# Optimization experiments

Hardware: AMD Instinct MI355X
Metric: run time of the kernel (lower is better)

## Reference

```python
import jax, jax.numpy as jnp
import numpy as np

K = 3  # PyG TAGConv default number of hops


def _gcn_norm(edge_index, num_nodes):
    # Symmetric GCN normalization WITHOUT self-loops (TAGConv default).
    row, col = edge_index[0], edge_index[1]
    w = jnp.ones(edge_index.shape[1], dtype=jnp.float32)
    deg = jax.ops.segment_sum(w, col, num_segments=num_nodes)
    dinv = jnp.where(deg > 0, jax.lax.rsqrt(jnp.maximum(deg, 1.0)), 0.0)
    return dinv[row] * dinv[col]  # [E]


def _tagconv(x, edge_index, norm, W, b):
    # W: [K+1, d_in, d_out], b: [d_out]
    row, col = edge_index[0], edge_index[1]
    n = x.shape[0]
    out = x @ W[0]
    h = x
    for k in range(1, K + 1):
        # h <- D^-1/2 A D^-1/2 h  via gather + segment-sum scatter
        h = jax.ops.segment_sum(norm[:, None] * h[row], col, num_segments=n)
        out = out + h @ W[k]
    return out + b


def setup_inputs() -> dict:
    key = jax.random.key(0)
    k1, k2, k3, k4, k5, k6 = jax.random.split(key, 6)
    N, E = 100000, 1600000
    d_in, d_hid, d_out = 64, 64, 40
    x = jax.random.normal(k1, (N, d_in), dtype=jnp.float32)
    edge_index = jax.random.randint(k2, (2, E), 0, N, dtype=jnp.int32)
    s1 = 1.0 / np.sqrt(d_in)
    s2 = 1.0 / np.sqrt(d_hid)
    W1 = jax.random.uniform(k3, (K + 1, d_in, d_hid), jnp.float32, -s1, s1)
    b1 = jnp.zeros((d_hid,), jnp.float32)
    W2 = jax.random.uniform(k4, (K + 1, d_hid, d_out), jnp.float32, -s2, s2)
    b2 = jnp.zeros((d_out,), jnp.float32)
    return {"x": x, "edge_index": edge_index, "W1": W1, "b1": b1, "W2": W2, "b2": b2}


def reference(x, edge_index, W1, b1, W2, b2):
    norm = _gcn_norm(edge_index, x.shape[0])
    h = jax.nn.relu(_tagconv(x, edge_index, norm, W1, b1))
    # F.dropout in eval mode: identity
    h = _tagconv(h, edge_index, norm, W2, b2)
    return jax.nn.log_softmax(h, axis=1)
```

## Files before the change

### kernel.cpp

```cpp
#include <hip/hip_runtime.h>
#include <math.h>

#define DIN 64
#define NB_MAX 512
#define S1_CHUNK 4096

typedef unsigned short us8 __attribute__((ext_vector_type(8)));
typedef short s16x8 __attribute__((ext_vector_type(8)));
typedef float f32x4 __attribute__((ext_vector_type(4)));


__device__ __forceinline__ float bf2f(unsigned short u) {
    return __uint_as_float(((unsigned int)u) << 16);
}
__device__ __forceinline__ unsigned short f2bf(float f) {
    unsigned int u = __float_as_uint(f);
    return (unsigned short)((u + 0x7fffu + ((u >> 16) & 1u)) >> 16);
}


__global__ __launch_bounds__(256) void bcount_kernel(const int* __restrict__ col,
                                                     int* __restrict__ bcnt, int E, int NB) {
    __shared__ int cntB[NB_MAX];
    for (int t = threadIdx.x; t < NB; t += 256) cntB[t] = 0;
    __syncthreads();
    int stride = gridDim.x * blockDim.x;
    for (int i = blockIdx.x * blockDim.x + threadIdx.x; i < E; i += stride)
        atomicAdd(&cntB[col[i] >> 8], 1);
    __syncthreads();
    for (int t = threadIdx.x; t < NB; t += 256) {
        int c = cntB[t];
        if (c) atomicAdd(&bcnt[t], c);
    }
}

__global__ void bscan_kernel(const int* __restrict__ bcnt, int* __restrict__ bbase,
                             int* __restrict__ gcur, int* __restrict__ rowptr,
                             int NB, int N, int E) {
    __shared__ int sm[512];
    int tid = threadIdx.x;
    int v = (tid < NB) ? bcnt[tid] : 0;
    sm[tid] = v;
    __syncthreads();
    for (int off = 1; off < 512; off <<= 1) {
        int add = (tid >= off) ? sm[tid - off] : 0;
        __syncthreads();
        sm[tid] += add;
        __syncthreads();
    }
    if (tid < NB) { int b = sm[tid] - v; bbase[tid] = b; gcur[tid] = b; }
    if (tid == NB - 1) bbase[NB] = sm[tid];
    if (tid == 0) rowptr[N] = E;
}


__global__ __launch_bounds__(256) void s1_bucket(const int* __restrict__ row,
                                                 const int* __restrict__ col,
                                                 int* __restrict__ gcur,
                                                 int* __restrict__ sorted, int E, int NB) {
    __shared__ int2 ebuf[S1_CHUNK];
    __shared__ int cntL[NB_MAX];
    __shared__ int baseL[NB_MAX];
    __shared__ int curL[NB_MAX];
    __shared__ int gbaseL[NB_MAX];
    __shared__ int sm[256];
    int tid = threadIdx.x;
    int jb = blockIdx.x * S1_CHUNK;
    int je = min(jb + S1_CHUNK, E);
    int cntTot = je - jb;

    for (int t = tid; t < NB; t += 256) cntL[t] = 0;
    __syncthreads();
    for (int j = jb + tid; j < je; j += 256) atomicAdd(&cntL[col[j] >> 8], 1);
    __syncthreads();
    int per = (NB + 255) >> 8;
    int s = 0;
    for (int q = 0; q < per; ++q) {
        int idx = tid * per + q;
        if (idx < NB) s += cntL[idx];
    }
    sm[tid] = s;
    __syncthreads();
    for (int off = 1; off < 256; off <<= 1) {
        int add = (tid >= off) ? sm[tid - off] : 0;
        __syncthreads();
        sm[tid] += add;
        __syncthreads();
    }
    int run = sm[tid] - s;
    for (int q = 0; q < per; ++q) {
        int idx = tid * per + q;
        if (idx < NB) { baseL[idx] = run; curL[idx] = run; run += cntL[idx]; }
    }
    __syncthreads();
    for (int t = tid; t < NB; t += 256)
        gbaseL[t] = atomicAdd(&gcur[t], cntL[t]);
    for (int j = jb + tid; j < je; j += 256) {
        int c = col[j];
        int pos = atomicAdd(&curL[c >> 8], 1);
        ebuf[pos] = make_int2(row[j], c);
    }
    __syncthreads();
    for (int jj = tid; jj < cntTot; jj += 256) {
        int2 e = ebuf[jj];
        int t = e.y >> 8;
        sorted[gbaseL[t] + (jj - baseL[t])] = (e.x << 8) | (e.y & 255);
    }
}


__global__ __launch_bounds__(256) void s2_kernel(const int* __restrict__ sorted,
                                                 const int* __restrict__ bbase,
                                                 int* __restrict__ rowptr,
                                                 float* __restrict__ dinv,
                                                 float* __restrict__ rdinv,
                                                 int* __restrict__ srcarr, int N) {
    __shared__ int cntL[256], baseL[256], sm[256];
    int tid = threadIdx.x;
    int b = blockIdx.x;
    int c0 = b << 8;
    int nLoc = min(256, N - c0);
    int gs = bbase[b], ge = bbase[b + 1];
    cntL[tid] = 0;
    __syncthreads();
    for (int j = gs + tid; j < ge; j += 256)
        atomicAdd(&cntL[sorted[j] & 255], 1);
    __syncthreads();
    int c = cntL[tid];
    sm[tid] = c;
    __syncthreads();
    for (int off = 1; off < 256; off <<= 1) {
        int add = (tid >= off) ? sm[tid - off] : 0;
        __syncthreads();
        sm[tid] += add;
        __syncthreads();
    }
    int base = gs + sm[tid] - c;
    baseL[tid] = base;
    if (tid < nLoc) {
        rowptr[c0 + tid] = base;
        dinv[c0 + tid] = (c > 0) ? rsqrtf((float)c) : 0.0f;
        rdinv[c0 + tid] = (c > 0) ? sqrtf((float)c) : 0.0f;
    }
    cntL[tid] = 0;
    __syncthreads();
    for (int j = gs + tid; j < ge; j += 256) {
        int e = sorted[j];
        int cl = e & 255;
        int p = baseL[cl] + atomicAdd(&cntL[cl], 1);
        srcarr[p] = e >> 8;
    }
}


__global__ void cvt_kernel(const float* __restrict__ x, const float* __restrict__ dinv,
                           unsigned short* __restrict__ hb0, unsigned short* __restrict__ sb0,
                           int n4) {
    int i = blockIdx.x * blockDim.x + threadIdx.x;
    if (i >= n4) return;
    float d = dinv[i >> 4];
    float4 v = *(const float4*)&x[(size_t)i * 4];
    ushort4 h, s;
    h.x = f2bf(v.x); h.y = f2bf(v.y); h.z = f2bf(v.z); h.w = f2bf(v.w);
    s.x = f2bf(d * v.x); s.y = f2bf(d * v.y); s.z = f2bf(d * v.z); s.w = f2bf(d * v.w);
    *(ushort4*)&hb0[(size_t)i * 4] = h;
    *(ushort4*)&sb0[(size_t)i * 4] = s;
}


__global__ __launch_bounds__(256) void prop_kernel(const int* __restrict__ rowptr,
                                                   const int* __restrict__ srcarr,
                                                   const float* __restrict__ dinv,
                                                   const unsigned short* __restrict__ sb_in,
                                                   unsigned short* __restrict__ sb_out, int N) {
    int gid = blockIdx.x * blockDim.x + threadIdx.x;
    int node = gid >> 6;
    if (node >= N) return;
    int lane = threadIdx.x & 63;
    int g = lane >> 3, l = lane & 7;
    int beg = rowptr[node], end = rowptr[node + 1];
    int deg = end - beg;
    float a[8] = {};
    for (int chunk = 0; chunk < deg; chunk += 64) {
        int lim = min(64, deg - chunk);
        int src_l = (lane < lim) ? srcarr[beg + chunk + lane] : 0;
        int iters = (lim + 7) >> 3;
        for (int t = 0; t < iters; ++t) {
            int jj = g + (t << 3);
            int src = __shfl(src_l, jj, 64);
            if (jj < lim) {
                us8 hv = *(const us8*)&sb_in[(size_t)src * DIN + l * 8];
#pragma unroll
                for (int k = 0; k < 8; ++k) a[k] += bf2f(hv[k]);
            }
        }
    }
#pragma unroll
    for (int off = 8; off < 64; off <<= 1) {
#pragma unroll
        for (int k = 0; k < 8; ++k) a[k] += __shfl_xor(a[k], off, 64);
    }
    if (g == 0) {
        float d = dinv[node];
        float d2 = d * d;
        us8 o;
#pragma unroll
        for (int k = 0; k < 8; ++k) o[k] = f2bf(d2 * a[k]);
        *(us8*)&sb_out[(size_t)node * DIN + l * 8] = o;
    }
}


__global__ void wprep_kernel(const float* __restrict__ W, unsigned short* __restrict__ Wb,
                             int DOUTsrc, int CT) {
    int idx = blockIdx.x * blockDim.x + threadIdx.x;
    int total = 4 * 2 * CT * 64;
    if (idx >= total) return;
    int lane = idx & 63;
    int rest = idx >> 6;
    int ct = rest % CT;
    int tmp = rest / CT;
    int ks = tmp & 1, kk = tmp >> 1;
    int colc = ct * 16 + (lane & 15);
    int k0 = ks * 32 + (lane >> 4) * 8;
    us8 ov;
#pragma unroll
    for (int j = 0; j < 8; ++j) {
        float v = (colc < DOUTsrc) ? W[(size_t)(kk * 64 + k0 + j) * DOUTsrc + colc] : 0.0f;
        ov[j] = f2bf(v);
    }
    *(us8*)&Wb[(size_t)idx * 8] = ov;
}


template <int CT, int MODE>
__global__ __launch_bounds__(256) void mm4m_kernel(const unsigned short* __restrict__ h0,
                                                   const unsigned short* __restrict__ s1,
                                                   const unsigned short* __restrict__ s2,
                                                   const unsigned short* __restrict__ s3,
                                                   const float* __restrict__ rdinv,
                                                   const float* __restrict__ dinv,
                                                   const unsigned short* __restrict__ Wb,
                                                   const float* __restrict__ bias,
                                                   float* __restrict__ outf,
                                                   unsigned short* __restrict__ outh,
                                                   unsigned short* __restrict__ outs, int N) {
    constexpr int LSTR = (MODE == 2) ? 68 : 52;
    __shared__ __align__(16) float Lds[64 * LSTR];
    int tid = threadIdx.x;
    int w = tid >> 6, lane = tid & 63;
    int row0 = blockIdx.x * 64 + w * 16;
    int arow = row0 + (lane & 15);
    bool aok = arow < N;
    size_t abase = (size_t)arow * DIN + ((lane >> 4) * 8);
    const unsigned short* hp[4] = {h0, s1, s2, s3};

    f32x4 acc0[CT] = {};
    f32x4 accS[CT] = {};
#pragma unroll
    for (int kk = 0; kk < 4; ++kk) {
        const unsigned short* hb = hp[kk];
#pragma unroll
        for (int ks = 0; ks < 2; ++ks) {
            s16x8 a = {};
            if (aok) a = *(const s16x8*)&hb[abase + ks * 32];
#pragma unroll
            for (int c = 0; c < CT; ++c) {
                s16x8 b = *(const s16x8*)&Wb[(size_t)(((kk * 2 + ks) * CT + c) * 64 + lane) * 8];
                if (kk == 0)
                    acc0[c] = __builtin_amdgcn_mfma_f32_16x16x32_bf16(a, b, acc0[c], 0, 0, 0);
                else
                    accS[c] = __builtin_amdgcn_mfma_f32_16x16x32_bf16(a, b, accS[c], 0, 0, 0);
            }
        }
    }
    int lcol = lane & 15;
    int lrow4 = (lane >> 4) * 4;
#pragma unroll
    for (int r = 0; r < 4; ++r) {
        int lr = lrow4 + r;
        int grow = row0 + lr;
        float rd = (grow < N) ? rdinv[grow] : 0.0f;
#pragma unroll
        for (int c = 0; c < CT; ++c) {
            float v = acc0[c][r] + rd * accS[c][r];
            if (MODE == 2) {
                v += bias[c * 16 + lcol];
                v = v > 0.0f ? v : 0.0f;
            }
            Lds[(w * 16 + lr) * LSTR + c * 16 + lcol] = v;
        }
    }
    __syncthreads();
    int rowsInBlk = min(64, N - blockIdx.x * 64);
    if (MODE == 2) {
        for (int idx = tid; idx < rowsInBlk * 8; idx += 256) {
            int r = idx >> 3, k8 = (idx & 7) * 8;
            int gr = blockIdx.x * 64 + r;
            float d = dinv[gr];
            us8 oh, os;
#pragma unroll
            for (int k = 0; k < 8; ++k) {
                float v = Lds[r * LSTR + k8 + k];
                oh[k] = f2bf(v);
                os[k] = f2bf(d * v);
            }
            *(us8*)&outh[(size_t)gr * DIN + k8] = oh;
            *(us8*)&outs[(size_t)gr * DIN + k8] = os;
        }
    } else {
        for (int idx = tid; idx < rowsInBlk * 10; idx += 256) {
            int r = idx / 10, c4 = idx - r * 10;
            int gr = blockIdx.x * 64 + r;
            float4 v = *(float4*)&Lds[r * LSTR + c4 * 4];
            *(float4*)&outf[(size_t)gr * 40 + c4 * 4] = v;
        }
    }
}


__global__ void lsm_kernel(float* __restrict__ out, const float* __restrict__ bias, int N) {
    int gid = blockIdx.x * blockDim.x + threadIdx.x;
    int row = gid >> 6;
    int lane = gid & 63;
    if (row >= N) return;
    float v = (lane < 40) ? out[(size_t)row * 40 + lane] + bias[lane] : -INFINITY;
    float m = v;
    for (int off = 32; off > 0; off >>= 1) m = fmaxf(m, __shfl_xor(m, off, 64));
    float e = (lane < 40) ? expf(v - m) : 0.0f;
    float ssum = e;
    for (int off = 32; off > 0; off >>= 1) ssum += __shfl_xor(ssum, off, 64);
    if (lane < 40) out[(size_t)row * 40 + lane] = v - m - logf(ssum);
}


extern "C" void kernel_launch(void* const* d_in, const int* in_sizes, int n_in,
                              void* d_out, int out_size, void* d_ws, size_t ws_size,
                              hipStream_t stream) {
    const float* x  = (const float*)d_in[0];
    const int*   ei = (const int*)d_in[1];
    const float* W1 = (const float*)d_in[2];
    const float* b1 = (const float*)d_in[3];
    const float* W2 = (const float*)d_in[4];
    const float* b2 = (const float*)d_in[5];

    int N = in_sizes[0] / DIN;
    int E = in_sizes[1] / 2;
    const int* rowv = ei;
    const int* colv = ei + E;
    int NB = (N + 255) >> 8;

    char* p = (char*)d_ws;
    auto alloc = [&](size_t bytes) {
        char* q = p;
        p += (bytes + 255) & ~(size_t)255;
        return q;
    };
    int*   bcnt   = (int*)alloc(NB_MAX * 4);
    int*   bbase  = (int*)alloc((NB_MAX + 1) * 4);
    int*   gcur   = (int*)alloc(NB_MAX * 4);
    int*   rowptr = (int*)alloc((size_t)(N + 1) * 4);
    float* dinv   = (float*)alloc((size_t)N * 4);
    float* rdinv  = (float*)alloc((size_t)N * 4);
    int*   sorted = (int*)alloc((size_t)E * 4);
    int*   srcarr = (int*)alloc((size_t)E * 4);
    unsigned short* Wb1 = (unsigned short*)alloc((size_t)4 * 2 * 4 * 64 * 8 * 2);
    unsigned short* Wb2 = (unsigned short*)alloc((size_t)4 * 2 * 3 * 64 * 8 * 2);
    unsigned short* hb0 = (unsigned short*)alloc((size_t)N * DIN * 2);
    unsigned short* hbE = (unsigned short*)alloc((size_t)N * DIN * 2);
    unsigned short* sbA = (unsigned short*)alloc((size_t)N * DIN * 2);
    unsigned short* sbB = (unsigned short*)alloc((size_t)N * DIN * 2);
    unsigned short* sbC = (unsigned short*)alloc((size_t)N * DIN * 2);
    unsigned short* sbD = (unsigned short*)alloc((size_t)N * DIN * 2);
    float* outp   = (float*)d_out;

    hipMemsetAsync(bcnt, 0, NB_MAX * 4, stream);

    const int tpb = 256;

    bcount_kernel<<<128, tpb, 0, stream>>>(colv, bcnt, E, NB);
    bscan_kernel<<<1, 512, 0, stream>>>(bcnt, bbase, gcur, rowptr, NB, N, E);
    s1_bucket<<<(E + S1_CHUNK - 1) / S1_CHUNK, 256, 0, stream>>>(rowv, colv, gcur, sorted, E, NB);
    s2_kernel<<<NB, 256, 0, stream>>>(sorted, bbase, rowptr, dinv, rdinv, srcarr, N);
    wprep_kernel<<<8, tpb, 0, stream>>>(W1, Wb1, 64, 4);
    wprep_kernel<<<6, tpb, 0, stream>>>(W2, Wb2, 40, 3);

    int propBlocks = (N * 64 + tpb - 1) / tpb;
    int mmBlocks = (N + 63) / 64;
    int n4 = N * 16;
    cvt_kernel<<<(n4 + tpb - 1) / tpb, tpb, 0, stream>>>(x, dinv, hb0, sbA, n4);

    prop_kernel<<<propBlocks, tpb, 0, stream>>>(rowptr, srcarr, dinv, sbA, sbB, N);
    prop_kernel<<<propBlocks, tpb, 0, stream>>>(rowptr, srcarr, dinv, sbB, sbC, N);
    prop_kernel<<<propBlocks, tpb, 0, stream>>>(rowptr, srcarr, dinv, sbC, sbD, N);
    mm4m_kernel<4, 2><<<mmBlocks, 256, 0, stream>>>(hb0, sbB, sbC, sbD, rdinv, dinv,
                                                    Wb1, b1, nullptr, hbE, sbA, N);

    prop_kernel<<<propBlocks, tpb, 0, stream>>>(rowptr, srcarr, dinv, sbA, sbB, N);
    prop_kernel<<<propBlocks, tpb, 0, stream>>>(rowptr, srcarr, dinv, sbB, sbC, N);
    prop_kernel<<<propBlocks, tpb, 0, stream>>>(rowptr, srcarr, dinv, sbC, sbD, N);
    mm4m_kernel<3, 0><<<mmBlocks, 256, 0, stream>>>(hbE, sbB, sbC, sbD, rdinv, dinv,
                                                    Wb2, nullptr, outp, nullptr, nullptr, N);

    lsm_kernel<<<propBlocks, tpb, 0, stream>>>(outp, b2, N);
}
```

Measured before the change: 393.1 us.

## Reorder second TAGConv layer to project before propagation, using Horner form

The second layer now multiplies the hidden features by all four weight slices first, producing 40-wide projections. It then runs three propagations over these 40-wide bf16 rows in Horner form, adding the next projection at each step, instead of propagating 64-wide rows and projecting afterwards. The aim is to cut gather traffic in the memory-bound sparse propagation from 64 to 40 columns per edge. The final log-softmax folds in the last propagated term and the bias. This costs extra intermediate buffers and a separate matmul kernel, and accumulating in bf16 across the Horner steps may shift rounding.

```diff
diff --git a/kernel.cpp b/kernel.cpp
--- a/kernel.cpp
+++ b/kernel.cpp
@@ -211,6 +211,57 @@
 }
 
 
+template <bool ADDIN>
+__global__ __launch_bounds__(256) void prop40_kernel(const int* __restrict__ rowptr,
+                                                     const int* __restrict__ srcarr,
+                                                     const float* __restrict__ dinv,
+                                                     const unsigned short* __restrict__ in,
+                                                     const unsigned short* __restrict__ addin,
+                                                     unsigned short* __restrict__ out, int N) {
+    int gid = blockIdx.x * blockDim.x + threadIdx.x;
+    int node = gid >> 6;
+    if (node >= N) return;
+    int lane = threadIdx.x & 63;
+    int g = lane >> 3, l = lane & 7;
+    int beg = rowptr[node], end = rowptr[node + 1];
+    int deg = end - beg;
+    float a[8] = {};
+    for (int chunk = 0; chunk < deg; chunk += 64) {
+        int lim = min(64, deg - chunk);
+        int src_l = (lane < lim) ? srcarr[beg + chunk + lane] : 0;
+        int iters = (lim + 7) >> 3;
+        for (int t = 0; t < iters; ++t) {
+            int jj = g + (t << 3);
+            int src = __shfl(src_l, jj, 64);
+            if (jj < lim && l < 5) {
+                us8 hv = *(const us8*)&in[(size_t)src * 40 + l * 8];
+#pragma unroll
+                for (int k = 0; k < 8; ++k) a[k] += bf2f(hv[k]);
+            }
+        }
+    }
+#pragma unroll
+    for (int off = 8; off < 64; off <<= 1) {
+#pragma unroll
+        for (int k = 0; k < 8; ++k) a[k] += __shfl_xor(a[k], off, 64);
+    }
+    if (g == 0 && l < 5) {
+        float d = dinv[node];
+        float d2 = d * d;
+        us8 o;
+        if (ADDIN) {
+            us8 ad = *(const us8*)&addin[(size_t)node * 40 + l * 8];
+#pragma unroll
+            for (int k = 0; k < 8; ++k) o[k] = f2bf(bf2f(ad[k]) + d2 * a[k]);
+        } else {
+#pragma unroll
+            for (int k = 0; k < 8; ++k) o[k] = f2bf(d2 * a[k]);
+        }
+        *(us8*)&out[(size_t)node * 40 + l * 8] = o;
+    }
+}
+
+
 __global__ void wprep_kernel(const float* __restrict__ W, unsigned short* __restrict__ Wb,
                              int DOUTsrc, int CT) {
     int idx = blockIdx.x * blockDim.x + threadIdx.x;
@@ -297,16 +348,17 @@
         for (int idx = tid; idx < rowsInBlk * 8; idx += 256) {
             int r = idx >> 3, k8 = (idx & 7) * 8;
             int gr = blockIdx.x * 64 + r;
-            float d = dinv[gr];
-            us8 oh, os;
-#pragma unroll
-            for (int k = 0; k < 8; ++k) {
-                float v = Lds[r * LSTR + k8 + k];
-                oh[k] = f2bf(v);
-                os[k] = f2bf(d * v);
-            }
+            us8 oh;
+#pragma unroll
+            for (int k = 0; k < 8; ++k) oh[k] = f2bf(Lds[r * LSTR + k8 + k]);
             *(us8*)&outh[(size_t)gr * DIN + k8] = oh;
-            *(us8*)&outs[(size_t)gr * DIN + k8] = os;
+            if (outs != nullptr) {
+                float d = dinv[gr];
+                us8 os;
+#pragma unroll
+                for (int k = 0; k < 8; ++k) os[k] = f2bf(d * Lds[r * LSTR + k8 + k]);
+                *(us8*)&outs[(size_t)gr * DIN + k8] = os;
+            }
         }
     } else {
         for (int idx = tid; idx < rowsInBlk * 10; idx += 256) {
@@ -319,12 +371,84 @@
 }
 
 
-__global__ void lsm_kernel(float* __restrict__ out, const float* __restrict__ bias, int N) {
+__global__ __launch_bounds__(256) void mmU_kernel(const unsigned short* __restrict__ P,
+                                                  const float* __restrict__ dinv,
+                                                  const unsigned short* __restrict__ Wb,
+                                                  float* __restrict__ u0f,
+                                                  unsigned short* __restrict__ u1,
+                                                  unsigned short* __restrict__ u2,
+                                                  unsigned short* __restrict__ u3, int N) {
+    constexpr int CT = 3, LSTR = 52;
+    __shared__ __align__(16) float Lds[64 * LSTR];
+    int tid = threadIdx.x;
+    int w = tid >> 6, lane = tid & 63;
+    int row0 = blockIdx.x * 64 + w * 16;
+    int arow = row0 + (lane & 15);
+    bool aok = arow < N;
+    size_t abase = (size_t)arow * DIN + ((lane >> 4) * 8);
+    s16x8 a0 = {}, a1 = {};
+    if (aok) {
+        a0 = *(const s16x8*)&P[abase];
+        a1 = *(const s16x8*)&P[abase + 32];
+    }
+    f32x4 acc[4][CT] = {};
+#pragma unroll
+    for (int kk = 0; kk < 4; ++kk) {
+#pragma unroll
+        for (int c = 0; c < CT; ++c) {
+            s16x8 b0 = *(const s16x8*)&Wb[(size_t)(((kk * 2 + 0) * CT + c) * 64 + lane) * 8];
+            s16x8 b1 = *(const s16x8*)&Wb[(size_t)(((kk * 2 + 1) * CT + c) * 64 + lane) * 8];
+            acc[kk][c] = __builtin_amdgcn_mfma_f32_16x16x32_bf16(a0, b0, acc[kk][c], 0, 0, 0);
+            acc[kk][c] = __builtin_amdgcn_mfma_f32_16x16x32_bf16(a1, b1, acc[kk][c], 0, 0, 0);
+        }
+    }
+    int lcol = lane & 15;
+    int lrow4 = (lane >> 4) * 4;
+    int rowsInBlk = min(64, N - blockIdx.x * 64);
+    unsigned short* up[4] = {nullptr, u1, u2, u3};
+#pragma unroll
+    for (int kk = 0; kk < 4; ++kk) {
+#pragma unroll
+        for (int r = 0; r < 4; ++r)
+#pragma unroll
+            for (int c = 0; c < CT; ++c)
+                Lds[(w * 16 + lrow4 + r) * LSTR + c * 16 + lcol] = acc[kk][c][r];
+        __syncthreads();
+        if (kk == 0) {
+            for (int idx = tid; idx < rowsInBlk * 10; idx += 256) {
+                int r = idx / 10, c4 = idx - r * 10;
+                int gr = blockIdx.x * 64 + r;
+                float4 v = *(float4*)&Lds[r * LSTR + c4 * 4];
+                *(float4*)&u0f[(size_t)gr * 40 + c4 * 4] = v;
+            }
+        } else {
+            unsigned short* u = up[kk];
+            for (int idx = tid; idx < rowsInBlk * 5; idx += 256) {
+                int r = idx / 5, seg = idx - r * 5;
+                int gr = blockIdx.x * 64 + r;
+                float d = dinv[gr];
+                us8 o;
+#pragma unroll
+                for (int k = 0; k < 8; ++k) o[k] = f2bf(d * Lds[r * LSTR + seg * 8 + k]);
+                *(us8*)&u[(size_t)gr * 40 + seg * 8] = o;
+            }
+        }
+        __syncthreads();
+    }
+}
+
+
+__global__ void lsm_kernel(float* __restrict__ out, const unsigned short* __restrict__ t,
+                           const float* __restrict__ rdinv, const float* __restrict__ bias,
+                           int N) {
     int gid = blockIdx.x * blockDim.x + threadIdx.x;
     int row = gid >> 6;
     int lane = gid & 63;
     if (row >= N) return;
-    float v = (lane < 40) ? out[(size_t)row * 40 + lane] + bias[lane] : -INFINITY;
+    float rd = rdinv[row];
+    float v = -INFINITY;
+    if (lane < 40)
+        v = out[(size_t)row * 40 + lane] + rd * bf2f(t[(size_t)row * 40 + lane]) + bias[lane];
     float m = v;
     for (int off = 32; off > 0; off >>= 1) m = fmaxf(m, __shfl_xor(m, off, 64));
     float e = (lane < 40) ? expf(v - m) : 0.0f;
@@ -372,6 +496,11 @@
     unsigned short* sbB = (unsigned short*)alloc((size_t)N * DIN * 2);
     unsigned short* sbC = (unsigned short*)alloc((size_t)N * DIN * 2);
     unsigned short* sbD = (unsigned short*)alloc((size_t)N * DIN * 2);
+    unsigned short* u1  = (unsigned short*)alloc((size_t)N * 40 * 2);
+    unsigned short* u2  = (unsigned short*)alloc((size_t)N * 40 * 2);
+    unsigned short* u3  = (unsigned short*)alloc((size_t)N * 40 * 2);
+    unsigned short* t40A = (unsigned short*)alloc((size_t)N * 40 * 2);
+    unsigned short* t40B = (unsigned short*)alloc((size_t)N * 40 * 2);
     float* outp   = (float*)d_out;
 
     hipMemsetAsync(bcnt, 0, NB_MAX * 4, stream);
@@ -394,13 +523,11 @@
     prop_kernel<<<propBlocks, tpb, 0, stream>>>(rowptr, srcarr, dinv, sbB, sbC, N);
     prop_kernel<<<propBlocks, tpb, 0, stream>>>(rowptr, srcarr, dinv, sbC, sbD, N);
     mm4m_kernel<4, 2><<<mmBlocks, 256, 0, stream>>>(hb0, sbB, sbC, sbD, rdinv, dinv,
-                                                    Wb1, b1, nullptr, hbE, sbA, N);
-
-    prop_kernel<<<propBlocks, tpb, 0, stream>>>(rowptr, srcarr, dinv, sbA, sbB, N);
-    prop_kernel<<<propBlocks, tpb, 0, stream>>>(rowptr, srcarr, dinv, sbB, sbC, N);
-    prop_kernel<<<propBlocks, tpb, 0, stream>>>(rowptr, srcarr, dinv, sbC, sbD, N);
-    mm4m_kernel<3, 0><<<mmBlocks, 256, 0, stream>>>(hbE, sbB, sbC, sbD, rdinv, dinv,
-                                                    Wb2, nullptr, outp, nullptr, nullptr, N);
-
-    lsm_kernel<<<propBlocks, tpb, 0, stream>>>(outp, b2, N);
-}
+                                                    Wb1, b1, nullptr, hbE, nullptr, N);
+
+    mmU_kernel<<<mmBlocks, 256, 0, stream>>>(hbE, dinv, Wb2, outp, u1, u2, u3, N);
+    prop40_kernel<true><<<propBlocks, tpb, 0, stream>>>(rowptr, srcarr, dinv, u3, u2, t40A, N);
+    prop40_kernel<true><<<propBlocks, tpb, 0, stream>>>(rowptr, srcarr, dinv, t40A, u1, t40B, N);
+    prop40_kernel<false><<<propBlocks, tpb, 0, stream>>>(rowptr, srcarr, dinv, t40B, nullptr, t40A, N);
+    lsm_kernel<<<propBlocks, tpb, 0, stream>>>(outp, t40A, rdinv, b2, N);
+}
```

Result: no change. 394.5 us (+0.4%).
